# Kernel optimization log

Measured on AMD Instinct MI355X. Metric: run time of the kernel, lower is better.

Reference implementation:

```python
import jax, jax.numpy as jnp
import numpy as np

DIM_EMB = 1024
DIM_K = 128
DIM_V = 128
BATCH = 4
SEQ = 4096

def setup_inputs() -> dict:
    key = jax.random.key(0)
    kx, kq, kk, kv = jax.random.split(key, 4)
    x = jax.random.normal(kx, (BATCH, SEQ, DIM_EMB), dtype=jnp.float32)
    Wq = jax.random.normal(kq, (DIM_EMB, DIM_K), dtype=jnp.float32) * (1.0 / np.sqrt(DIM_EMB))
    Wk = jax.random.normal(kk, (DIM_EMB, DIM_K), dtype=jnp.float32) * (1.0 / np.sqrt(DIM_EMB))
    Wv = jax.random.normal(kv, (DIM_EMB, DIM_V), dtype=jnp.float32) * (1.0 / np.sqrt(DIM_EMB))
    return {"x": x, "Wq": Wq, "Wk": Wk, "Wv": Wv}

def reference(x, Wq, Wk, Wv):
    # x: [b, s, e]; projections (torch Linear without bias -> x @ W)
    seq_len = x.shape[1]
    q = x @ Wq  # [b, s, dk]
    k = x @ Wk  # [b, s, dk]
    v = x @ Wv  # [b, s, dv]
    # NOTE: original scales by 1/sqrt(dim_emb), not 1/sqrt(dim_k)
    scale = 1.0 / np.sqrt(x.shape[-1])
    qk = jnp.einsum('bqd,bkd->bqk', q, k) * scale  # [b, s, s]
    causal = jnp.tril(jnp.ones((seq_len, seq_len), dtype=bool))
    masked_qk = jnp.where(causal, qk, -jnp.inf)
    att = jax.nn.softmax(masked_qk, axis=-1)  # dropout p=0.0 -> identity
    return att @ v  # [b, s, dv]
```

## Files before the change

kernel.cpp:

```cpp
#include <hip/hip_runtime.h>

typedef __attribute__((ext_vector_type(8))) short s8v;
typedef __attribute__((ext_vector_type(4))) short s4v;
typedef __attribute__((ext_vector_type(4))) float f4v;

#define S_ 4096
#define E_ 1024
#define D_ 128

__device__ __forceinline__ unsigned short f2bf(float f) {
  unsigned int u = __float_as_uint(f);
  return (unsigned short)((u + 0x7FFFu + ((u >> 16) & 1u)) >> 16);
}

__device__ __forceinline__ void gload16(const void* g, void* l) {
  __builtin_amdgcn_global_load_lds(
      (const __attribute__((address_space(1))) unsigned int*)g,
      (__attribute__((address_space(3))) unsigned int*)l, 16, 0, 0);
}

__device__ __forceinline__ int slot_off(int s) { return s * (3840 - 256 * s); }

__global__ __launch_bounds__(256) void prep_kernel(
    const float* __restrict__ x, const float* __restrict__ Wq,
    const float* __restrict__ Wk, const float* __restrict__ Wv,
    unsigned short* __restrict__ Xb, unsigned short* __restrict__ Wt) {
  __shared__ unsigned short T[64][72];
  const int bid = blockIdx.x;
  if (bid < 8192) {
    const size_t i = ((size_t)bid * 256 + threadIdx.x) * 8;
    float4 a = *reinterpret_cast<const float4*>(x + i);
    float4 c = *reinterpret_cast<const float4*>(x + i + 4);
    s8v v;
    v[0] = (short)f2bf(a.x); v[1] = (short)f2bf(a.y);
    v[2] = (short)f2bf(a.z); v[3] = (short)f2bf(a.w);
    v[4] = (short)f2bf(c.x); v[5] = (short)f2bf(c.y);
    v[6] = (short)f2bf(c.z); v[7] = (short)f2bf(c.w);
    *reinterpret_cast<s8v*>(Xb + i) = v;
  } else {
    const int w = bid - 8192;
    const int p = w >> 5, bx = w & 31;
    const float* W = (p == 0) ? Wq : (p == 1) ? Wk : Wv;
    const int k0 = (bx >> 1) * 64;
    const int n0 = (bx & 1) * 64;
    const int t = threadIdx.x, rr = t >> 4, c4 = (t & 15) * 4;
#pragma unroll
    for (int i = 0; i < 4; ++i) {
      int kr = i * 16 + rr;
      float4 ww = *reinterpret_cast<const float4*>(W + (size_t)(k0 + kr) * D_ + n0 + c4);
      T[c4 + 0][kr] = f2bf(ww.x); T[c4 + 1][kr] = f2bf(ww.y);
      T[c4 + 2][kr] = f2bf(ww.z); T[c4 + 3][kr] = f2bf(ww.w);
    }
    __syncthreads();
#pragma unroll
    for (int i = 0; i < 4; ++i) {
      int n = i * 16 + rr;
      s4v v;
      v[0] = (short)T[n][c4]; v[1] = (short)T[n][c4 + 1];
      v[2] = (short)T[n][c4 + 2]; v[3] = (short)T[n][c4 + 3];
      *reinterpret_cast<s4v*>(Wt + (size_t)(p * D_ + n0 + n) * E_ + k0 + c4) = v;
    }
  }
}

__global__ __launch_bounds__(256) void proj_kernel(
    const unsigned short* __restrict__ Xb, const unsigned short* __restrict__ Wt,
    unsigned short* __restrict__ Qb, unsigned short* __restrict__ Kb,
    unsigned short* __restrict__ VT) {
  __shared__ __align__(16) unsigned short As[64 * 64];
  __shared__ __align__(16) unsigned short Bs[128 * 64];
  const int bid = blockIdx.x;
  const int cls = bid & 7, j = bid >> 3;
  const int m0 = (cls * 32 + j / 3) * 64, ng = j % 3;
  const int t = threadIdx.x;
  const int wv = t >> 6, lane = t & 63, quad = lane >> 4, l16 = lane & 15;
  const int wr = wv >> 1, wc = wv & 1;

  f4v acc[2][4];
  const f4v fz = {0.f, 0.f, 0.f, 0.f};
#pragma unroll
  for (int i = 0; i < 2; ++i)
#pragma unroll
    for (int k = 0; k < 4; ++k) acc[i][k] = fz;

  const int lrow = lane >> 3;
  const int scb = ((lane & 7) ^ lrow) * 16;
  const char* aSrc = (const char*)(Xb + (size_t)(m0 + wv * 16 + lrow) * E_) + scb;
  const char* bSrc = (const char*)(Wt + (size_t)(ng * 128 + wv * 32 + lrow) * E_) + scb;

  const int xm = (l16 & 7) * 16;
  const char* Ab = (const char*)As + (wr * 32 + l16) * 128;
  const char* Bb = (const char*)Bs + (wc * 64 + l16) * 128;

  for (int kk = 0; kk < E_; kk += 64) {
#pragma unroll
    for (int i = 0; i < 2; ++i)
      gload16(aSrc + (size_t)(i * 8 * E_ + kk) * 2, (char*)As + wv * 2048 + i * 1024);
#pragma unroll
    for (int i = 0; i < 4; ++i)
      gload16(bSrc + (size_t)(i * 8 * E_ + kk) * 2, (char*)Bs + wv * 4096 + i * 1024);
    __syncthreads();
#pragma unroll
    for (int ks = 0; ks < 2; ++ks) {
      const int co = (ks * 64 + quad * 16) ^ xm;
      s8v af[2], bf[4];
#pragma unroll
      for (int rt = 0; rt < 2; ++rt)
        af[rt] = *reinterpret_cast<const s8v*>(Ab + rt * 2048 + co);
#pragma unroll
      for (int ct = 0; ct < 4; ++ct)
        bf[ct] = *reinterpret_cast<const s8v*>(Bb + ct * 2048 + co);
#pragma unroll
      for (int rt = 0; rt < 2; ++rt)
#pragma unroll
        for (int ct = 0; ct < 4; ++ct)
          acc[rt][ct] = __builtin_amdgcn_mfma_f32_16x16x32_bf16(
              af[rt], bf[ct], acc[rt][ct], 0, 0, 0);
    }
    __syncthreads();
  }

  if (ng < 2) {
    unsigned short* dst = ng ? Kb : Qb;
#pragma unroll
    for (int rt = 0; rt < 2; ++rt)
#pragma unroll
      for (int ct = 0; ct < 4; ++ct)
#pragma unroll
        for (int r = 0; r < 4; ++r)
          dst[(size_t)(m0 + wr * 32 + rt * 16 + quad * 4 + r) * D_ +
              wc * 64 + ct * 16 + l16] = f2bf(acc[rt][ct][r]);
  } else {
    const int b = m0 >> 12;
    const int s0 = (m0 & (S_ - 1)) + wr * 32;
#pragma unroll
    for (int rt = 0; rt < 2; ++rt)
#pragma unroll
      for (int ct = 0; ct < 4; ++ct) {
        s4v v;
        v[0] = (short)f2bf(acc[rt][ct][0]); v[1] = (short)f2bf(acc[rt][ct][1]);
        v[2] = (short)f2bf(acc[rt][ct][2]); v[3] = (short)f2bf(acc[rt][ct][3]);
        *reinterpret_cast<s4v*>(
            VT + ((size_t)b * D_ + wc * 64 + ct * 16 + l16) * S_ + s0 +
            rt * 16 + quad * 4) = v;
      }
  }
}

__global__ __launch_bounds__(256, 4) void flash_kernel(
    const unsigned short* __restrict__ Qb, const unsigned short* __restrict__ Kb,
    const unsigned short* __restrict__ VT, float* __restrict__ Op,
    float* __restrict__ Lp) {
  __shared__ __align__(16) unsigned short KS[64 * 128];
  __shared__ __align__(16) unsigned short VS[128 * 72];
  const int id = blockIdx.x;
  const int xcd = id & 7;
  const int b = xcd >> 1;
  const int sub = 287 - ((id >> 3) * 2 + (xcd & 1));
  int g = 0;
#pragma unroll
  for (int gg = 0; gg < 7; ++gg)
    if (sub >= 4 * (gg + 1) * (gg + 2)) g = gg + 1;
  const int off = sub - 4 * g * (g + 1);
  const int qt = 8 * g + off / (g + 1);
  const int s = off % (g + 1);
  const int q0 = qt * 64;
  const int klo = s * 512;
  const int khi = min((s + 1) * 512, (qt + 1) * 64);

  const int t = threadIdx.x;
  const int wv = t >> 6, lane = t & 63, quad = lane >> 4, l16 = lane & 15;
  const int qrow0 = q0 + wv * 16;
  const float SCL2 = 0.03125f * 1.44269504088896340736f;

  const unsigned short* Kbb = Kb + (size_t)b * S_ * D_;
  const unsigned short* Vbb = VT + (size_t)b * D_ * S_;

  s8v Qf[4];
#pragma unroll
  for (int ks = 0; ks < 4; ++ks)
    Qf[ks] = *reinterpret_cast<const s8v*>(
        Qb + ((size_t)b * S_ + qrow0 + l16) * D_ + ks * 32 + quad * 8);

  f4v O[8];
  const f4v fz = {0.f, 0.f, 0.f, 0.f};
#pragma unroll
  for (int nt = 0; nt < 8; ++nt) O[nt] = fz;
  float lt = 0.f;

  const int krow = t >> 4, kgb = t & 15;
  const int vrow = t >> 1, vgb = (t & 1) * 4;

  s8v kr[4], vr[4];
#pragma unroll
  for (int i = 0; i < 4; ++i) {
    kr[i] = *reinterpret_cast<const s8v*>(
        Kbb + (size_t)(klo + krow + 16 * i) * D_ + kgb * 8);
    vr[i] = *reinterpret_cast<const s8v*>(
        Vbb + (size_t)vrow * S_ + klo + (vgb + i) * 8);
  }

  for (int k0 = klo; k0 < khi; k0 += 64) {
    __syncthreads();
#pragma unroll
    for (int i = 0; i < 4; ++i) {
      const int r = krow + 16 * i;
      const int sig = (krow & 3) | ((((krow >> 3) + 2 * i) & 3) << 2);
      *reinterpret_cast<s8v*>(KS + r * 128 + ((kgb ^ sig) * 8)) = kr[i];
      *reinterpret_cast<s8v*>(VS + vrow * 72 + (vgb + i) * 8) = vr[i];
    }
    __syncthreads();
    if (k0 + 64 < khi) {
#pragma unroll
      for (int i = 0; i < 4; ++i) {
        kr[i] = *reinterpret_cast<const s8v*>(
            Kbb + (size_t)(k0 + 64 + krow + 16 * i) * D_ + kgb * 8);
        vr[i] = *reinterpret_cast<const s8v*>(
            Vbb + (size_t)vrow * S_ + k0 + 64 + (vgb + i) * 8);
      }
    }

    if (k0 <= qrow0 + 15) {
      f4v St[2][2];
#pragma unroll
      for (int c = 0; c < 2; ++c)
#pragma unroll
        for (int s2 = 0; s2 < 2; ++s2) St[c][s2] = fz;
      __builtin_amdgcn_s_setprio(1);
#pragma unroll
      for (int ks = 0; ks < 4; ++ks)
#pragma unroll
        for (int c = 0; c < 2; ++c)
#pragma unroll
          for (int s2 = 0; s2 < 2; ++s2) {
            const int row = c * 32 + ((l16 >> 2) << 3) + s2 * 4 + (l16 & 3);
            s8v kf = *reinterpret_cast<const s8v*>(
                KS + row * 128 + (((ks * 4 + quad) ^ l16) * 8));
            St[c][s2] = __builtin_amdgcn_mfma_f32_16x16x32_bf16(
                kf, Qf[ks], St[c][s2], 0, 0, 0);
          }
      __builtin_amdgcn_s_setprio(0);
      const bool full = (k0 + 63 <= qrow0);
      s8v pf[2];
#pragma unroll
      for (int c = 0; c < 2; ++c) {
        float ladd = 0.f;
#pragma unroll
        for (int s2 = 0; s2 < 2; ++s2)
#pragma unroll
          for (int r = 0; r < 4; ++r) {
            float e = exp2f(St[c][s2][r] * SCL2);
            if (!full) {
              int key = k0 + c * 32 + quad * 8 + s2 * 4 + r;
              if (key > qrow0 + l16) e = 0.f;
            }
            ladd += e;
            pf[c][s2 * 4 + r] = (short)f2bf(e);
          }
        lt += ladd;
      }
      __builtin_amdgcn_s_setprio(1);
#pragma unroll
      for (int c = 0; c < 2; ++c)
#pragma unroll
        for (int nt = 0; nt < 8; ++nt) {
          s8v vf = *reinterpret_cast<const s8v*>(
              VS + (nt * 16 + l16) * 72 + (c * 4 + quad) * 8);
          O[nt] = __builtin_amdgcn_mfma_f32_16x16x32_bf16(
              pf[c], vf, O[nt], 0, 0, 0);
        }
      __builtin_amdgcn_s_setprio(0);
    }
  }

  lt += __shfl_xor(lt, 16);
  lt += __shfl_xor(lt, 32);
  const int soff = slot_off(s);
#pragma unroll
  for (int nt = 0; nt < 8; ++nt)
#pragma unroll
    for (int r = 0; r < 4; ++r)
      Op[((size_t)(qrow0 + quad * 4 + r + soff) * 4 + b) * D_ + nt * 16 + l16] =
          O[nt][r];
  if (lane < 16) Lp[(size_t)(qrow0 + l16 + soff) * 4 + b] = lt;
}

__global__ __launch_bounds__(256) void norm_kernel(
    const float* __restrict__ Op, const float* __restrict__ Lp,
    float* __restrict__ out) {
  const int idx = blockIdx.x * 256 + threadIdx.x;
  const int rowg = idx >> 5, d4 = idx & 31;
  const int b = rowg >> 12, row = rowg & 4095;
  const int g = row >> 9;
  float ax = 0.f, ay = 0.f, az = 0.f, aw = 0.f, L = 0.f;
  for (int s = 0; s <= g; ++s) {
    const size_t pr = (size_t)(row + slot_off(s)) * 4 + b;
    float4 o = reinterpret_cast<const float4*>(Op + pr * D_)[d4];
    ax += o.x; ay += o.y; az += o.z; aw += o.w;
    L += Lp[pr];
  }
  float4 r;
  const float inv = 1.f / L;
  r.x = ax * inv; r.y = ay * inv; r.z = az * inv; r.w = aw * inv;
  reinterpret_cast<float4*>(out)[idx] = r;
}

extern "C" void kernel_launch(void* const* d_in, const int* in_sizes, int n_in,
                              void* d_out, int out_size, void* d_ws, size_t ws_size,
                              hipStream_t stream) {
  const float* x = (const float*)d_in[0];
  const float* Wq = (const float*)d_in[1];
  const float* Wk = (const float*)d_in[2];
  const float* Wv = (const float*)d_in[3];
  float* out = (float*)d_out;

  char* ws = (char*)d_ws;
  unsigned short* Qb = (unsigned short*)ws;
  unsigned short* Kb = (unsigned short*)(ws + (((size_t)4) << 20));
  unsigned short* VT = (unsigned short*)(ws + (((size_t)8) << 20));
  unsigned short* Wt = (unsigned short*)(ws + (((size_t)12) << 20));
  unsigned short* Xb = (unsigned short*)(ws + (((size_t)13) << 20));
  float* Op = (float*)(ws + (((size_t)13) << 20));
  float* Lp = (float*)(ws + (((size_t)50) << 20));

  prep_kernel<<<8288, 256, 0, stream>>>(x, Wq, Wk, Wv, Xb, Wt);
  proj_kernel<<<768, 256, 0, stream>>>(Xb, Wt, Qb, Kb, VT);
  flash_kernel<<<1152, 256, 0, stream>>>(Qb, Kb, VT, Op, Lp);
  norm_kernel<<<2048, 256, 0, stream>>>(Op, Lp, out);
}
```

Measured before the change: 171.4 us.

## Fuse split-K normalization into flash kernel via last-block atomic counter

Removes the separate norm kernel. Each flash block now increments a per-(batch, query-tile) counter, and the last of the split blocks to finish reduces the partial outputs and sums and writes the normalized result. A counter reset is added to the prep kernel as an extra block. The bf16 conversion of probabilities also switches to the HIP intrinsic. This saves a kernel launch and the extra pass over partials, at the cost of threadfences and a serialized tail reduction in the last-arriving block.

Result: slower. 274.7 us (+60.3%).

```diff
diff --git a/kernel.cpp b/kernel.cpp
--- a/kernel.cpp
+++ b/kernel.cpp
@@ -1,4 +1,5 @@
 #include <hip/hip_runtime.h>
+#include <hip/hip_bf16.h>
 
 typedef __attribute__((ext_vector_type(8))) short s8v;
 typedef __attribute__((ext_vector_type(4))) short s4v;
@@ -11,6 +12,12 @@
 __device__ __forceinline__ unsigned short f2bf(float f) {
   unsigned int u = __float_as_uint(f);
   return (unsigned short)((u + 0x7FFFu + ((u >> 16) & 1u)) >> 16);
+}
+
+__device__ __forceinline__ unsigned short f2bf_c(float f) {
+  union { __hip_bfloat16 h; unsigned short u; } cv;
+  cv.h = __float2bfloat16(f);
+  return cv.u;
 }
 
 __device__ __forceinline__ void gload16(const void* g, void* l) {
@@ -24,7 +31,8 @@
 __global__ __launch_bounds__(256) void prep_kernel(
     const float* __restrict__ x, const float* __restrict__ Wq,
     const float* __restrict__ Wk, const float* __restrict__ Wv,
-    unsigned short* __restrict__ Xb, unsigned short* __restrict__ Wt) {
+    unsigned short* __restrict__ Xb, unsigned short* __restrict__ Wt,
+    int* __restrict__ cnt) {
   __shared__ unsigned short T[64][72];
   const int bid = blockIdx.x;
   if (bid < 8192) {
@@ -37,7 +45,7 @@
     v[4] = (short)f2bf(c.x); v[5] = (short)f2bf(c.y);
     v[6] = (short)f2bf(c.z); v[7] = (short)f2bf(c.w);
     *reinterpret_cast<s8v*>(Xb + i) = v;
-  } else {
+  } else if (bid < 8288) {
     const int w = bid - 8192;
     const int p = w >> 5, bx = w & 31;
     const float* W = (p == 0) ? Wq : (p == 1) ? Wk : Wv;
@@ -60,6 +68,8 @@
       v[2] = (short)T[n][c4 + 2]; v[3] = (short)T[n][c4 + 3];
       *reinterpret_cast<s4v*>(Wt + (size_t)(p * D_ + n0 + n) * E_ + k0 + c4) = v;
     }
+  } else {
+    cnt[threadIdx.x] = 0;
   }
 }
 
@@ -150,7 +160,7 @@
 __global__ __launch_bounds__(256, 4) void flash_kernel(
     const unsigned short* __restrict__ Qb, const unsigned short* __restrict__ Kb,
     const unsigned short* __restrict__ VT, float* __restrict__ Op,
-    float* __restrict__ Lp) {
+    float* __restrict__ Lp, float* __restrict__ out, int* __restrict__ cnt) {
   __shared__ __align__(16) unsigned short KS[64 * 128];
   __shared__ __align__(16) unsigned short VS[128 * 72];
   const int id = blockIdx.x;
@@ -255,7 +265,7 @@
               if (key > qrow0 + l16) e = 0.f;
             }
             ladd += e;
-            pf[c][s2 * 4 + r] = (short)f2bf(e);
+            pf[c][s2 * 4 + r] = (short)f2bf_c(e);
           }
         lt += ladd;
       }
@@ -283,26 +293,33 @@
       Op[((size_t)(qrow0 + quad * 4 + r + soff) * 4 + b) * D_ + nt * 16 + l16] =
           O[nt][r];
   if (lane < 16) Lp[(size_t)(qrow0 + l16 + soff) * 4 + b] = lt;
-}
-
-__global__ __launch_bounds__(256) void norm_kernel(
-    const float* __restrict__ Op, const float* __restrict__ Lp,
-    float* __restrict__ out) {
-  const int idx = blockIdx.x * 256 + threadIdx.x;
-  const int rowg = idx >> 5, d4 = idx & 31;
-  const int b = rowg >> 12, row = rowg & 4095;
-  const int g = row >> 9;
-  float ax = 0.f, ay = 0.f, az = 0.f, aw = 0.f, L = 0.f;
-  for (int s = 0; s <= g; ++s) {
-    const size_t pr = (size_t)(row + slot_off(s)) * 4 + b;
-    float4 o = reinterpret_cast<const float4*>(Op + pr * D_)[d4];
-    ax += o.x; ay += o.y; az += o.z; aw += o.w;
-    L += Lp[pr];
-  }
-  float4 r;
-  const float inv = 1.f / L;
-  r.x = ax * inv; r.y = ay * inv; r.z = az * inv; r.w = aw * inv;
-  reinterpret_cast<float4*>(out)[idx] = r;
+
+  __syncthreads();
+  int* flag = (int*)KS;
+  if (t == 0) {
+    __threadfence();
+    *flag = (atomicAdd(&cnt[b * 64 + qt], 1) == g) ? 1 : 0;
+  }
+  __syncthreads();
+  if (*flag) {
+    __threadfence();
+    const int c4 = t & 31;
+#pragma unroll
+    for (int p = 0; p < 8; ++p) {
+      const int r = q0 + p * 8 + (t >> 5);
+      float4 a = {0.f, 0.f, 0.f, 0.f};
+      float L = 0.f;
+      for (int s2 = 0; s2 <= g; ++s2) {
+        const size_t pr = (size_t)(r + slot_off(s2)) * 4 + b;
+        float4 o = reinterpret_cast<const float4*>(Op + pr * D_)[c4];
+        a.x += o.x; a.y += o.y; a.z += o.z; a.w += o.w;
+        L += Lp[pr];
+      }
+      const float inv = 1.f / L;
+      float4 w = {a.x * inv, a.y * inv, a.z * inv, a.w * inv};
+      reinterpret_cast<float4*>(out + ((size_t)b * S_ + r) * D_)[c4] = w;
+    }
+  }
 }
 
 extern "C" void kernel_launch(void* const* d_in, const int* in_sizes, int n_in,
@@ -322,9 +339,9 @@
   unsigned short* Xb = (unsigned short*)(ws + (((size_t)13) << 20));
   float* Op = (float*)(ws + (((size_t)13) << 20));
   float* Lp = (float*)(ws + (((size_t)50) << 20));
-
-  prep_kernel<<<8288, 256, 0, stream>>>(x, Wq, Wk, Wv, Xb, Wt);
+  int* cnt = (int*)(ws + (((size_t)51) << 20));
+
+  prep_kernel<<<8289, 256, 0, stream>>>(x, Wq, Wk, Wv, Xb, Wt, cnt);
   proj_kernel<<<768, 256, 0, stream>>>(Xb, Wt, Qb, Kb, VT);
-  flash_kernel<<<1152, 256, 0, stream>>>(Qb, Kb, VT, Op, Lp);
-  norm_kernel<<<2048, 256, 0, stream>>>(Op, Lp, out);
-}
+  flash_kernel<<<1152, 256, 0, stream>>>(Qb, Kb, VT, Op, Lp, out, cnt);
+}
```
